# Performance work log

Hardware: AMD Instinct MI355X
Metric: run time of the kernel (lower is better)

## Reference

```python
import jax, jax.numpy as jnp
import numpy as np

EPS = 1e-7


def ciou_pairwise(b1, b2):
    # b1: (N,1,4), b2: (1,N,4) in xyxy; returns (N,N) CIoU
    b1x1, b1y1, b1x2, b1y2 = b1[..., 0], b1[..., 1], b1[..., 2], b1[..., 3]
    b2x1, b2y1, b2x2, b2y2 = b2[..., 0], b2[..., 1], b2[..., 2], b2[..., 3]

    # intersection
    iw = jnp.clip(jnp.minimum(b1x2, b2x2) - jnp.maximum(b1x1, b2x1), 0.0)
    ih = jnp.clip(jnp.minimum(b1y2, b2y2) - jnp.maximum(b1y1, b2y1), 0.0)
    inter = iw * ih

    w1, h1 = b1x2 - b1x1, b1y2 - b1y1
    w2, h2 = b2x2 - b2x1, b2y2 - b2y1
    union = w1 * h1 + w2 * h2 - inter + EPS
    iou = inter / union

    # smallest enclosing box diagonal
    cw = jnp.maximum(b1x2, b2x2) - jnp.minimum(b1x1, b2x1)
    ch = jnp.maximum(b1y2, b2y2) - jnp.minimum(b1y1, b2y1)
    c2 = cw * cw + ch * ch + EPS

    # squared center distance
    rho2 = ((b2x1 + b2x2 - b1x1 - b1x2) ** 2 + (b2y1 + b2y2 - b1y1 - b1y2) ** 2) / 4.0

    # aspect-ratio consistency term
    v = (4.0 / (np.pi ** 2)) * (jnp.arctan(w2 / (h2 + EPS)) - jnp.arctan(w1 / (h1 + EPS))) ** 2
    alpha = jax.lax.stop_gradient(v / (v - iou + (1.0 + EPS)))
    return iou - (rho2 / c2 + v * alpha)


def setup_inputs() -> dict:
    key = jax.random.key(0)
    k1, k2, k3 = jax.random.split(key, 3)
    N = 4096
    conf = jax.random.uniform(k1, (N, 1), dtype=jnp.float32)           # confidence in [0,1)
    xy1 = jax.random.uniform(k2, (N, 2), dtype=jnp.float32) * 600.0    # top-left corner
    wh = jax.random.uniform(k3, (N, 2), dtype=jnp.float32) * 100.0 + 1.0  # width/height >= 1
    x = jnp.concatenate([conf, xy1, xy1 + wh], axis=1)                 # (N, 5): conf, x1, y1, x2, y2
    gamma = jnp.zeros((1,), dtype=jnp.float32)
    return {"x": x, "gamma": gamma}


def reference(x, gamma):
    boxes = x[:, 1:]
    conf = x[:, 0]
    iou = ciou_pairwise(boxes[:, None, :], boxes[None, :, :])          # (N, N)
    conf_matrix = conf[:, None] * conf[None, :]                        # (N, N) outer product
    attention = jax.nn.softmax(iou * conf_matrix, axis=-1)             # (N, N)
    x_prime = x * gamma + attention @ x                                # (N, 5)
    return jax.nn.sigmoid(x_prime)
```

## Files before the change

kernel.cpp:

```cpp
#include <hip/hip_runtime.h>
#include <math.h>

#define N 4096
#define FEPS 1e-7f
#define BLK 256
#define JT 64
#define CH (N / JT)
#define LSTRIDE 12
#define N6 (N * 6)


__device__ __forceinline__ void box_record(const float* __restrict__ x, int i, float* rec) {
    float cf = x[i * 5 + 0], x1 = x[i * 5 + 1], y1 = x[i * 5 + 2];
    float x2 = x[i * 5 + 3], y2 = x[i * 5 + 4];
    float w = x2 - x1, h = y2 - y1;
    rec[0] = cf; rec[1] = x1; rec[2] = y1; rec[3] = x2; rec[4] = y2;
    rec[5] = (x1 + x2) * 0.5f; rec[6] = (y1 + y2) * 0.5f; rec[7] = w; rec[8] = h;
    rec[9] = w * h + 0.5f * FEPS;
    rec[10] = 0.6366197723675814f * atanf(w / (h + FEPS));
    rec[11] = cf * 1.2011224087864498f;
}

__global__ __launch_bounds__(BLK) void ciou_attn_kernel(
        const float* __restrict__ x,
        float* __restrict__ part) {
    __shared__ float jrec[CH * LSTRIDE];
    const int tid = threadIdx.x;
    const int gb = blockIdx.x / JT;
    const int jt = blockIdx.x % JT;
    const int i = gb * BLK + tid;

    if (tid < CH) box_record(x, jt * CH + tid, &jrec[tid * LSTRIDE]);

    float R[12];
    box_record(x, i, R);
    const float rx1 = R[1], ry1 = R[2], rx2 = R[3], ry2 = R[4];
    const float rhx = R[5], rhy = R[6], rw = R[7], rh = R[8];
    const float rareps = R[9], rat = R[10], rcf2 = R[11];

    __syncthreads();

    float sum = 0.f, a0 = 0.f, a1 = 0.f, a2 = 0.f, a3 = 0.f, a4 = 0.f;
    const float ONEP = 1.f + FEPS;

#pragma unroll 4
    for (int jj = 0; jj < CH; jj++) {
        const float* fj = &jrec[jj * LSTRIDE];
        float jcf = fj[0], jx1 = fj[1], jy1 = fj[2], jx2 = fj[3], jy2 = fj[4];
        float jhx = fj[5], jhy = fj[6], jw = fj[7], jh = fj[8];
        float jareps = fj[9], jat = fj[10], jcf2 = fj[11];

        float iwr = fminf(rx2, jx2) - fmaxf(rx1, jx1);
        float ihr = fminf(ry2, jy2) - fmaxf(ry1, jy1);
        float iw = fmaxf(iwr, 0.f);
        float ih = fmaxf(ihr, 0.f);
        float inter = iw * ih;
        float uni = (rareps + jareps) - inter;
        float iou = fminf(inter * __builtin_amdgcn_rcpf(uni), 1.0f);
        float cw = (rw + jw) - iwr;
        float ch = (rh + jh) - ihr;
        float c2 = fmaf(cw, cw, fmaf(ch, ch, FEPS));
        float dx = jhx - rhx;
        float dy = jhy - rhy;
        float rho2 = fmaf(dx, dx, dy * dy);
        float da = jat - rat;
        float v = da * da;
        float den = (v - iou) + ONEP;
        float valpha = (v * v) * __builtin_amdgcn_rcpf(den);
        float ciou = iou - fmaf(rho2, __builtin_amdgcn_rcpf(c2), valpha);
        float e = __builtin_amdgcn_exp2f(ciou * (rcf2 * jcf2));
        sum += e;
        a0 = fmaf(e, jcf, a0);
        a1 = fmaf(e, jx1, a1);
        a2 = fmaf(e, jy1, a2);
        a3 = fmaf(e, jx2, a3);
        a4 = fmaf(e, jy2, a4);
    }

    float* p = part + (size_t)jt * N6 + (size_t)i * 6;
    p[0] = sum; p[1] = a0; p[2] = a1; p[3] = a2; p[4] = a3; p[5] = a4;
}

__global__ void epilogue_kernel(const float* __restrict__ x,
                                const float* __restrict__ gamma,
                                const float* __restrict__ part,
                                float* __restrict__ out) {
    int idx = blockIdx.x * blockDim.x + threadIdx.x;
    if (idx >= N * 5) return;
    int i = idx / 5, c = idx % 5;
    float se = 0.f, a = 0.f;
    const float* p = part + (size_t)i * 6;
#pragma unroll 8
    for (int jt = 0; jt < JT; jt++) {
        se += p[jt * (size_t)N6 + 0];
        a  += p[jt * (size_t)N6 + 1 + c];
    }
    float xp = x[idx] * gamma[0] + a / se;
    out[idx] = 1.f / (1.f + expf(-xp));
}

extern "C" void kernel_launch(void* const* d_in, const int* in_sizes, int n_in,
                              void* d_out, int out_size, void* d_ws, size_t ws_size,
                              hipStream_t stream) {
    const float* x = (const float*)d_in[0];
    const float* gamma = (const float*)d_in[1];
    float* out = (float*)d_out;
    float* part = (float*)d_ws;

    ciou_attn_kernel<<<(N / BLK) * JT, BLK, 0, stream>>>(x, part);
    epilogue_kernel<<<(N * 5 + 255) / 256, 256, 0, stream>>>(x, gamma, part, out);
}
```

Before: 83.92 us.

## Merge CIoU reciprocals into one rcp and pack j-records as float4 with prefetch

Rewrites the per-pair CIoU so its three reciprocals (union, enclosing diagonal, alpha denominator) become a single reciprocal of a combined denominator. The numerator is formed algebraically, which cuts transcendental-unit work in the inner loop. The shared-memory j-records are repacked as three float4s and the next record is software-prefetched into registers, reducing LDS instructions and hiding their latency. The combined product of terms risks precision loss or overflow, and the iou clamp to 1 is dropped.

```diff
diff --git a/kernel.cpp b/kernel.cpp
--- a/kernel.cpp
+++ b/kernel.cpp
@@ -3,78 +3,92 @@
 
 #define N 4096
 #define FEPS 1e-7f
+#define HEPS 5e-8f
 #define BLK 256
 #define JT 64
 #define CH (N / JT)
-#define LSTRIDE 12
 #define N6 (N * 6)
+#define KATAN 0.6366197723675814f
+#define SQL2E 1.2011224087864498f
 
-
-__device__ __forceinline__ void box_record(const float* __restrict__ x, int i, float* rec) {
-    float cf = x[i * 5 + 0], x1 = x[i * 5 + 1], y1 = x[i * 5 + 2];
-    float x2 = x[i * 5 + 3], y2 = x[i * 5 + 4];
-    float w = x2 - x1, h = y2 - y1;
-    rec[0] = cf; rec[1] = x1; rec[2] = y1; rec[3] = x2; rec[4] = y2;
-    rec[5] = (x1 + x2) * 0.5f; rec[6] = (y1 + y2) * 0.5f; rec[7] = w; rec[8] = h;
-    rec[9] = w * h + 0.5f * FEPS;
-    rec[10] = 0.6366197723675814f * atanf(w / (h + FEPS));
-    rec[11] = cf * 1.2011224087864498f;
-}
 
 __global__ __launch_bounds__(BLK) void ciou_attn_kernel(
         const float* __restrict__ x,
         float* __restrict__ part) {
-    __shared__ float jrec[CH * LSTRIDE];
+    __shared__ float4 jrec[CH * 3];
     const int tid = threadIdx.x;
     const int gb = blockIdx.x / JT;
     const int jt = blockIdx.x % JT;
     const int i = gb * BLK + tid;
 
-    if (tid < CH) box_record(x, jt * CH + tid, &jrec[tid * LSTRIDE]);
+    if (tid < CH) {
+        int j = jt * CH + tid;
+        float cf = x[j * 5 + 0], jx1 = x[j * 5 + 1], jy1 = x[j * 5 + 2];
+        float jx2 = x[j * 5 + 3], jy2 = x[j * 5 + 4];
+        float w = jx2 - jx1, h = jy2 - jy1;
+        jrec[tid * 3 + 0] = make_float4(jx1, jy1, jx2, jy2);
+        jrec[tid * 3 + 1] = make_float4((jx1 + jx2) * 0.5f, (jy1 + jy2) * 0.5f, w, h);
+        jrec[tid * 3 + 2] = make_float4(fmaf(w, h, HEPS),
+                                        KATAN * atanf(w / (h + FEPS)),
+                                        cf * SQL2E, cf);
+    }
 
-    float R[12];
-    box_record(x, i, R);
-    const float rx1 = R[1], ry1 = R[2], rx2 = R[3], ry2 = R[4];
-    const float rhx = R[5], rhy = R[6], rw = R[7], rh = R[8];
-    const float rareps = R[9], rat = R[10], rcf2 = R[11];
+    {
+    }
+    float cfr = x[i * 5 + 0];
+    const float rx1 = x[i * 5 + 1], ry1 = x[i * 5 + 2];
+    const float rx2 = x[i * 5 + 3], ry2 = x[i * 5 + 4];
+    const float rw = rx2 - rx1, rh = ry2 - ry1;
+    const float rhx = (rx1 + rx2) * 0.5f, rhy = (ry1 + ry2) * 0.5f;
+    const float rareps = fmaf(rw, rh, HEPS);
+    const float rat = KATAN * atanf(rw / (rh + FEPS));
+    const float rcf2 = cfr * SQL2E;
 
     __syncthreads();
 
     float sum = 0.f, a0 = 0.f, a1 = 0.f, a2 = 0.f, a3 = 0.f, a4 = 0.f;
     const float ONEP = 1.f + FEPS;
 
+    float4 A = jrec[0], B = jrec[1], C = jrec[2];
 #pragma unroll 4
     for (int jj = 0; jj < CH; jj++) {
-        const float* fj = &jrec[jj * LSTRIDE];
-        float jcf = fj[0], jx1 = fj[1], jy1 = fj[2], jx2 = fj[3], jy2 = fj[4];
-        float jhx = fj[5], jhy = fj[6], jw = fj[7], jh = fj[8];
-        float jareps = fj[9], jat = fj[10], jcf2 = fj[11];
+        const int nx = ((jj + 1) & (CH - 1)) * 3;
+        float4 nA = jrec[nx + 0];
+        float4 nB = jrec[nx + 1];
+        float4 nC = jrec[nx + 2];
 
-        float iwr = fminf(rx2, jx2) - fmaxf(rx1, jx1);
-        float ihr = fminf(ry2, jy2) - fmaxf(ry1, jy1);
+        float iwr = fminf(rx2, A.z) - fmaxf(rx1, A.x);
+        float ihr = fminf(ry2, A.w) - fmaxf(ry1, A.y);
         float iw = fmaxf(iwr, 0.f);
         float ih = fmaxf(ihr, 0.f);
         float inter = iw * ih;
-        float uni = (rareps + jareps) - inter;
-        float iou = fminf(inter * __builtin_amdgcn_rcpf(uni), 1.0f);
-        float cw = (rw + jw) - iwr;
-        float ch = (rh + jh) - ihr;
-        float c2 = fmaf(cw, cw, fmaf(ch, ch, FEPS));
-        float dx = jhx - rhx;
-        float dy = jhy - rhy;
+        float uni = (rareps + C.x) - inter;
+        float cw = (rw + B.z) - iwr;
+        float chh = (rh + B.w) - ihr;
+        float c2 = fmaf(cw, cw, fmaf(chh, chh, FEPS));
+        float dx = B.x - rhx;
+        float dy = B.y - rhy;
         float rho2 = fmaf(dx, dx, dy * dy);
-        float da = jat - rat;
+        float da = C.y - rat;
         float v = da * da;
-        float den = (v - iou) + ONEP;
-        float valpha = (v * v) * __builtin_amdgcn_rcpf(den);
-        float ciou = iou - fmaf(rho2, __builtin_amdgcn_rcpf(c2), valpha);
-        float e = __builtin_amdgcn_exp2f(ciou * (rcf2 * jcf2));
+        float P = fmaf(v + ONEP, uni, -inter);
+        P = fmaxf(P, 1e-12f);
+        float uc = uni * c2;
+        float rr = __builtin_amdgcn_rcpf(uc * P);
+        float t1 = fmaf(inter, c2, -(rho2 * uni));
+        float vu = v * uni;
+        float n2 = (vu * vu) * c2;
+        float num = fmaf(t1, P, -n2);
+        float s = (num * rr) * (rcf2 * C.z);
+        float e = __builtin_amdgcn_exp2f(s);
         sum += e;
-        a0 = fmaf(e, jcf, a0);
-        a1 = fmaf(e, jx1, a1);
-        a2 = fmaf(e, jy1, a2);
-        a3 = fmaf(e, jx2, a3);
-        a4 = fmaf(e, jy2, a4);
+        a0 = fmaf(e, C.w, a0);
+        a1 = fmaf(e, A.x, a1);
+        a2 = fmaf(e, A.y, a2);
+        a3 = fmaf(e, A.z, a3);
+        a4 = fmaf(e, A.w, a4);
+
+        A = nA; B = nB; C = nC;
     }
 
     float* p = part + (size_t)jt * N6 + (size_t)i * 6;
```

New measurement: 83.70 us. Within noise of the previous version (-0.3%).

## Precompute box features, pack j-pairs for packed-FP32 math, merge reciprocals

Applied to the files above, without the earlier changes.

Adds a prepass kernel that computes per-box features once, in a row layout and in a j-pair-interleaved layout, so the main kernel no longer recomputes atan and the other derived terms per block. The inner loop handles two j boxes at a time with 2-wide float vectors, so the compiler can emit packed FP32 instructions. The CIoU expression is put over a common denominator, so three reciprocals become one. This adds a kernel launch and extra workspace, and changes numerics: the common-denominator product can overflow or lose precision, and the iou clamp is dropped.

```diff
diff --git a/kernel.cpp b/kernel.cpp
--- a/kernel.cpp
+++ b/kernel.cpp
@@ -3,82 +3,125 @@
 
 #define N 4096
 #define FEPS 1e-7f
+#define HEPS 5e-8f
 #define BLK 256
 #define JT 64
-#define CH (N / JT)
-#define LSTRIDE 12
+#define CH 64
+#define NPAIR (CH / 2)
 #define N6 (N * 6)
+#define KATAN 0.6366197723675814f
+#define SQL2E 1.2011224087864498f
+
+typedef float v2f __attribute__((ext_vector_type(2)));
 
 
-__device__ __forceinline__ void box_record(const float* __restrict__ x, int i, float* rec) {
+__global__ void feat_kernel(const float* __restrict__ x,
+                            float* __restrict__ feat_row,
+                            float* __restrict__ feat_pair) {
+    int i = blockIdx.x * blockDim.x + threadIdx.x;
+    if (i >= N) return;
     float cf = x[i * 5 + 0], x1 = x[i * 5 + 1], y1 = x[i * 5 + 2];
     float x2 = x[i * 5 + 3], y2 = x[i * 5 + 4];
     float w = x2 - x1, h = y2 - y1;
-    rec[0] = cf; rec[1] = x1; rec[2] = y1; rec[3] = x2; rec[4] = y2;
-    rec[5] = (x1 + x2) * 0.5f; rec[6] = (y1 + y2) * 0.5f; rec[7] = w; rec[8] = h;
-    rec[9] = w * h + 0.5f * FEPS;
-    rec[10] = 0.6366197723675814f * atanf(w / (h + FEPS));
-    rec[11] = cf * 1.2011224087864498f;
+    float rec[12];
+    rec[0] = x1; rec[1] = y1; rec[2] = x2; rec[3] = y2;
+    rec[4] = (x1 + x2) * 0.5f; rec[5] = (y1 + y2) * 0.5f;
+    rec[6] = w; rec[7] = h;
+    rec[8] = fmaf(w, h, HEPS);
+    rec[9] = KATAN * atanf(w / (h + FEPS));
+    rec[10] = cf * SQL2E; rec[11] = cf;
+    float4* dr = (float4*)(feat_row + (size_t)i * 12);
+    dr[0] = make_float4(rec[0], rec[1], rec[2], rec[3]);
+    dr[1] = make_float4(rec[4], rec[5], rec[6], rec[7]);
+    dr[2] = make_float4(rec[8], rec[9], rec[10], rec[11]);
+    float* dp = feat_pair + (size_t)(i >> 1) * 24 + (i & 1);
+#pragma unroll
+    for (int k = 0; k < 12; k++) dp[k * 2] = rec[k];
+}
+
+__device__ __forceinline__ v2f min2(v2f a, v2f b) {
+    v2f r; r.x = fminf(a.x, b.x); r.y = fminf(a.y, b.y); return r;
+}
+__device__ __forceinline__ v2f max2(v2f a, v2f b) {
+    v2f r; r.x = fmaxf(a.x, b.x); r.y = fmaxf(a.y, b.y); return r;
+}
+__device__ __forceinline__ v2f rcp2(v2f a) {
+    v2f r; r.x = __builtin_amdgcn_rcpf(a.x); r.y = __builtin_amdgcn_rcpf(a.y); return r;
+}
+__device__ __forceinline__ v2f exp22(v2f a) {
+    v2f r; r.x = __builtin_amdgcn_exp2f(a.x); r.y = __builtin_amdgcn_exp2f(a.y); return r;
 }
 
 __global__ __launch_bounds__(BLK) void ciou_attn_kernel(
-        const float* __restrict__ x,
+        const float* __restrict__ feat_row,
+        const float* __restrict__ feat_pair,
         float* __restrict__ part) {
-    __shared__ float jrec[CH * LSTRIDE];
+    __shared__ float jrec[NPAIR * 24];
     const int tid = threadIdx.x;
     const int gb = blockIdx.x / JT;
     const int jt = blockIdx.x % JT;
     const int i = gb * BLK + tid;
 
-    if (tid < CH) box_record(x, jt * CH + tid, &jrec[tid * LSTRIDE]);
+    if (tid < 192) {
+        ((float4*)jrec)[tid] =
+            ((const float4*)(feat_pair + (size_t)jt * NPAIR * 24))[tid];
+    }
 
-    float R[12];
-    box_record(x, i, R);
-    const float rx1 = R[1], ry1 = R[2], rx2 = R[3], ry2 = R[4];
-    const float rhx = R[5], rhy = R[6], rw = R[7], rh = R[8];
-    const float rareps = R[9], rat = R[10], rcf2 = R[11];
+    const float4* rp = (const float4*)(feat_row + (size_t)i * 12);
+    const float4 r0 = rp[0], r1 = rp[1], r2 = rp[2];
+    const float rx1 = r0.x, ry1 = r0.y, rx2 = r0.z, ry2 = r0.w;
+    const float rhx = r1.x, rhy = r1.y, rw = r1.z, rh = r1.w;
+    const float rareps = r2.x, rat = r2.y, rcf2 = r2.z;
 
     __syncthreads();
 
-    float sum = 0.f, a0 = 0.f, a1 = 0.f, a2 = 0.f, a3 = 0.f, a4 = 0.f;
+    v2f sum = 0.f, a0 = 0.f, a1 = 0.f, a2 = 0.f, a3 = 0.f, a4 = 0.f;
     const float ONEP = 1.f + FEPS;
 
 #pragma unroll 4
-    for (int jj = 0; jj < CH; jj++) {
-        const float* fj = &jrec[jj * LSTRIDE];
-        float jcf = fj[0], jx1 = fj[1], jy1 = fj[2], jx2 = fj[3], jy2 = fj[4];
-        float jhx = fj[5], jhy = fj[6], jw = fj[7], jh = fj[8];
-        float jareps = fj[9], jat = fj[10], jcf2 = fj[11];
+    for (int p = 0; p < NPAIR; p++) {
+        const float* f = &jrec[p * 24];
+        const v2f X1 = *(const v2f*)(f + 0),  Y1 = *(const v2f*)(f + 2);
+        const v2f X2 = *(const v2f*)(f + 4),  Y2 = *(const v2f*)(f + 6);
+        const v2f HX = *(const v2f*)(f + 8),  HY = *(const v2f*)(f + 10);
+        const v2f W  = *(const v2f*)(f + 12), H  = *(const v2f*)(f + 14);
+        const v2f AR = *(const v2f*)(f + 16), AT = *(const v2f*)(f + 18);
+        const v2f CF2 = *(const v2f*)(f + 20), CF = *(const v2f*)(f + 22);
 
-        float iwr = fminf(rx2, jx2) - fmaxf(rx1, jx1);
-        float ihr = fminf(ry2, jy2) - fmaxf(ry1, jy1);
-        float iw = fmaxf(iwr, 0.f);
-        float ih = fmaxf(ihr, 0.f);
-        float inter = iw * ih;
-        float uni = (rareps + jareps) - inter;
-        float iou = fminf(inter * __builtin_amdgcn_rcpf(uni), 1.0f);
-        float cw = (rw + jw) - iwr;
-        float ch = (rh + jh) - ihr;
-        float c2 = fmaf(cw, cw, fmaf(ch, ch, FEPS));
-        float dx = jhx - rhx;
-        float dy = jhy - rhy;
-        float rho2 = fmaf(dx, dx, dy * dy);
-        float da = jat - rat;
-        float v = da * da;
-        float den = (v - iou) + ONEP;
-        float valpha = (v * v) * __builtin_amdgcn_rcpf(den);
-        float ciou = iou - fmaf(rho2, __builtin_amdgcn_rcpf(c2), valpha);
-        float e = __builtin_amdgcn_exp2f(ciou * (rcf2 * jcf2));
+        v2f iwr = min2(rx2, X2) - max2(rx1, X1);
+        v2f ihr = min2(ry2, Y2) - max2(ry1, Y1);
+        v2f inter = max2(iwr, 0.f) * max2(ihr, 0.f);
+        v2f uni = (rareps + AR) - inter;
+        v2f cw = (rw + W) - iwr;
+        v2f chh = (rh + H) - ihr;
+        v2f c2 = cw * cw + chh * chh + FEPS;
+        v2f dx = HX - rhx;
+        v2f dy = HY - rhy;
+        v2f rho2 = dx * dx + dy * dy;
+        v2f da = AT - rat;
+        v2f v = da * da;
+        v2f P = (v + ONEP) * uni - inter;
+        P = max2(P, 1e-12f);
+        v2f rr = rcp2(uni * c2 * P);
+        v2f t1 = inter * c2 - rho2 * uni;
+        v2f vu = v * uni;
+        v2f num = t1 * P - (vu * vu) * c2;
+        v2f e = exp22((num * rr) * (rcf2 * CF2));
         sum += e;
-        a0 = fmaf(e, jcf, a0);
-        a1 = fmaf(e, jx1, a1);
-        a2 = fmaf(e, jy1, a2);
-        a3 = fmaf(e, jx2, a3);
-        a4 = fmaf(e, jy2, a4);
+        a0 += e * CF;
+        a1 += e * X1;
+        a2 += e * Y1;
+        a3 += e * X2;
+        a4 += e * Y2;
     }
 
-    float* p = part + (size_t)jt * N6 + (size_t)i * 6;
-    p[0] = sum; p[1] = a0; p[2] = a1; p[3] = a2; p[4] = a3; p[5] = a4;
+    float* pp = part + (size_t)jt * N6 + (size_t)i * 6;
+    pp[0] = sum.x + sum.y;
+    pp[1] = a0.x + a0.y;
+    pp[2] = a1.x + a1.y;
+    pp[3] = a2.x + a2.y;
+    pp[4] = a3.x + a3.y;
+    pp[5] = a4.x + a4.y;
 }
 
 __global__ void epilogue_kernel(const float* __restrict__ x,
@@ -106,7 +149,10 @@
     const float* gamma = (const float*)d_in[1];
     float* out = (float*)d_out;
     float* part = (float*)d_ws;
+    float* feat_row = part + (size_t)JT * N6;
+    float* feat_pair = feat_row + (size_t)N * 12;
 
-    ciou_attn_kernel<<<(N / BLK) * JT, BLK, 0, stream>>>(x, part);
+    feat_kernel<<<(N + BLK - 1) / BLK, BLK, 0, stream>>>(x, feat_row, feat_pair);
+    ciou_attn_kernel<<<(N / BLK) * JT, BLK, 0, stream>>>(feat_row, feat_pair, part);
     epilogue_kernel<<<(N * 5 + 255) / 256, 256, 0, stream>>>(x, gamma, part, out);
 }
```

New measurement: 83.47 us. Within noise of the previous version (-0.5%).
